# Kernel tuning notes

Measured on AMD Instinct MI355X. Metric: run time of the kernel, lower is better.

Reference implementation:

```python
import jax, jax.numpy as jnp
import numpy as np
import math

D = 512
BT = 4096
N = 16
EPS = 1e-5

def layer_norm(x, g, b):
    mu = jnp.mean(x, axis=-1, keepdims=True)
    var = jnp.mean(jnp.square(x - mu), axis=-1, keepdims=True)
    return (x - mu) * jax.lax.rsqrt(var + EPS) * g + b

def setup_inputs() -> dict:
    key = jax.random.key(0)
    ks = jax.random.split(key, 8)
    x = jax.random.normal(ks[0], (BT, N, D), dtype=jnp.float32)
    # random bool mask (True = masked), but keep the diagonal unmasked so no
    # row is fully -inf (avoids NaN softmax, matching sane usage of the module)
    attn_mask = jax.random.randint(ks[1], (BT, N, N), 0, 2).astype(bool)
    eye = jnp.eye(N, dtype=bool)[None, :, :]
    attn_mask = jnp.where(eye, False, attn_mask)
    # LayerNorm params (torch init: weight=1, bias=0)
    g1 = jnp.ones((D,), jnp.float32); b1 = jnp.zeros((D,), jnp.float32)
    g2 = jnp.ones((D,), jnp.float32); b2 = jnp.zeros((D,), jnp.float32)
    # FFN params: Linear(D, 4D) then Linear(4D, D)
    s1 = 1.0 / math.sqrt(D)
    s2 = 1.0 / math.sqrt(4 * D)
    W1 = jax.random.uniform(ks[2], (D, 4 * D), jnp.float32, -s1, s1)
    bW1 = jax.random.uniform(ks[3], (4 * D,), jnp.float32, -s1, s1)
    W2 = jax.random.uniform(ks[4], (4 * D, D), jnp.float32, -s2, s2)
    bW2 = jax.random.uniform(ks[5], (D,), jnp.float32, -s2, s2)
    return {"x": x, "attn_mask": attn_mask, "g1": g1, "b1": b1,
            "g2": g2, "b2": b2, "W1": W1, "bW1": bW1, "W2": W2, "bW2": bW2}

def reference(x, attn_mask, g1, b1, g2, b2, W1, bW1, W2, bW2):
    d = x.shape[-1]
    # scores: [BT, N, N] = x x^T / sqrt(d)
    scores = jnp.einsum('bnd,bmd->bnm', x, x) / jnp.sqrt(jnp.asarray(d, x.dtype))
    scores = jnp.where(attn_mask, -jnp.inf, scores)
    attn = jax.nn.softmax(scores, axis=-1)
    out = jnp.einsum('bnm,bmd->bnd', attn, x)
    h = layer_norm(x + out, g1, b1)
    ff = jnp.maximum(h @ W1 + bW1, 0.0) @ W2 + bW2
    y = layer_norm(h + ff, g2, b2)
    return y, attn
```

## Files before the change

kernel.cpp:

```cpp
#include <hip/hip_runtime.h>

typedef float  f32x4 __attribute__((ext_vector_type(4)));
typedef short  short8 __attribute__((ext_vector_type(8)));

__device__ __forceinline__ unsigned short f2bf(float f) {
    unsigned u = __builtin_bit_cast(unsigned, f);
    unsigned r = u + 0x7FFFu + ((u >> 16) & 1u);
    return (unsigned short)(r >> 16);
}
__device__ __forceinline__ float bf2f(unsigned short b) {
    return __builtin_bit_cast(float, (unsigned)b << 16);
}

__device__ __forceinline__ f32x4 mfma16(short8 a, short8 b, f32x4 c) {
    return __builtin_amdgcn_mfma_f32_16x16x32_bf16(a, b, c, 0, 0, 0);
}

#define GLOAD16(gp, lp) \
    __builtin_amdgcn_global_load_lds((const __attribute__((address_space(1))) unsigned int*)(gp), \
                                     (__attribute__((address_space(3))) unsigned int*)(lp), 16, 0, 0)

#define BT   4096
#define NTOK 16
#define DDIM 512
#define Y_ELEMS 33554432ULL
#define XS_STRIDE 516

__global__ __launch_bounds__(256) void transpose_kernel(const float* __restrict__ in,
                                                        unsigned short* __restrict__ out,
                                                        int R, int C) {
    __shared__ float tile[32][33];
    const int tx = threadIdx.x & 31, ty = threadIdx.x >> 5;
    const int c0 = blockIdx.x * 32, r0 = blockIdx.y * 32;
#pragma unroll
    for (int i = 0; i < 4; ++i)
        tile[ty + 8 * i][tx] = in[(size_t)(r0 + ty + 8 * i) * C + c0 + tx];
    __syncthreads();
#pragma unroll
    for (int i = 0; i < 4; ++i)
        out[(size_t)(c0 + ty + 8 * i) * R + r0 + tx] = f2bf(tile[tx][ty + 8 * i]);
}

__global__ void detect_kernel(const unsigned char* __restrict__ m, int* __restrict__ flag) {
    __shared__ int any;
    if (threadIdx.x == 0) any = 0;
    __syncthreads();
    int loc = 0;
    for (int i = threadIdx.x; i < 4096; i += 256)
        if (i & 3) loc |= m[i];
    if (loc) atomicOr(&any, 1);
    __syncthreads();
    if (threadIdx.x == 0) *flag = any ? 1 : 0;
}

__global__ __launch_bounds__(256) void stage1_kernel(
    const float* __restrict__ x,
    const unsigned char* __restrict__ mask_u8, const int* __restrict__ mask_i32,
    const int* __restrict__ flagp,
    const float* __restrict__ g1, const float* __restrict__ b1,
    float* __restrict__ attn_out, unsigned short* __restrict__ hbf,
    float* __restrict__ hf32) {
    __shared__ float xs[NTOK * XS_STRIDE];
    __shared__ float p_lds[256];

    const int b = blockIdx.x, t = threadIdx.x;
    const float* xb = x + (size_t)b * (NTOK * DDIM);

#pragma unroll
    for (int i = 0; i < 8; ++i) {
        int s = t + 256 * i;
        int r = s >> 7, c4 = s & 127;
        f32x4 v = ((const f32x4*)xb)[s];
        *(f32x4*)(&xs[r * XS_STRIDE + c4 * 4]) = v;
    }
    __syncthreads();

    const int r = t >> 4, c = t & 15;
    {
        const f32x4* xr = (const f32x4*)(&xs[r * XS_STRIDE]);
        const f32x4* xc = (const f32x4*)(&xs[c * XS_STRIDE]);
        f32x4 d4 = {0.f, 0.f, 0.f, 0.f};
#pragma unroll 8
        for (int u = 0; u < 128; ++u) d4 += xr[u] * xc[u];
        float s_rc = (d4.x + d4.y + d4.z + d4.w) * 0.04419417382415922f;

        const int flag = *flagp;
        size_t midx = (size_t)b * 256 + t;
        bool msk = flag ? (mask_u8[midx] != 0) : (mask_i32[midx] != 0);
        float sv = msk ? -1e30f : s_rc;
        float mx = sv;
        mx = fmaxf(mx, __shfl_xor(mx, 1, 16));
        mx = fmaxf(mx, __shfl_xor(mx, 2, 16));
        mx = fmaxf(mx, __shfl_xor(mx, 4, 16));
        mx = fmaxf(mx, __shfl_xor(mx, 8, 16));
        float e = msk ? 0.f : expf(sv - mx);
        float sum = e;
        sum += __shfl_xor(sum, 1, 16);
        sum += __shfl_xor(sum, 2, 16);
        sum += __shfl_xor(sum, 4, 16);
        sum += __shfl_xor(sum, 8, 16);
        float p = e / sum;
        p_lds[t] = p;
        attn_out[midx] = p;
    }
    __syncthreads();

    const int r2 = t >> 4, tc = t & 15;
    f32x4 acc[8];
#pragma unroll
    for (int j = 0; j < 8; ++j) acc[j] = (f32x4){0.f, 0.f, 0.f, 0.f};
    for (int c2 = 0; c2 < 16; ++c2) {
        float pw = p_lds[r2 * 16 + c2];
        const f32x4* xrow = (const f32x4*)(&xs[c2 * XS_STRIDE]);
#pragma unroll
        for (int j = 0; j < 8; ++j) acc[j] += pw * xrow[tc + 16 * j];
    }

    const f32x4* xme = (const f32x4*)(&xs[r2 * XS_STRIDE]);
    f32x4 vv[8];
    float s1 = 0.f, s2 = 0.f;
#pragma unroll
    for (int j = 0; j < 8; ++j) {
        f32x4 v = xme[tc + 16 * j] + acc[j];
        vv[j] = v;
        s1 += v.x + v.y + v.z + v.w;
        s2 += v.x * v.x + v.y * v.y + v.z * v.z + v.w * v.w;
    }
    s1 += __shfl_xor(s1, 1, 16); s2 += __shfl_xor(s2, 1, 16);
    s1 += __shfl_xor(s1, 2, 16); s2 += __shfl_xor(s2, 2, 16);
    s1 += __shfl_xor(s1, 4, 16); s2 += __shfl_xor(s2, 4, 16);
    s1 += __shfl_xor(s1, 8, 16); s2 += __shfl_xor(s2, 8, 16);
    float mu = s1 * (1.f / 512.f);
    float var = s2 * (1.f / 512.f) - mu * mu;
    float inv = rsqrtf(var + 1e-5f);

    const size_t rowbase = (size_t)(b * NTOK + r2) * DDIM;
    unsigned short* hrow = hbf + rowbase;
    float* frow = hf32 + rowbase;
#pragma unroll
    for (int j = 0; j < 8; ++j) {
        int u = tc + 16 * j;
        f32x4 gv = ((const f32x4*)g1)[u];
        f32x4 bv = ((const f32x4*)b1)[u];
        f32x4 o = (vv[j] - mu) * inv * gv + bv;
        *(f32x4*)(frow + u * 4) = o;
        uint2 pk;
        pk.x = (unsigned)f2bf(o.x) | ((unsigned)f2bf(o.y) << 16);
        pk.y = (unsigned)f2bf(o.z) | ((unsigned)f2bf(o.w) << 16);
        *(uint2*)(hrow + u * 4) = pk;
    }
}


#define PH_READA(Al, Q) { short8 a00, a01, a10, a11; \
    a00 = *(const short8*)((Al) + aoffs[2*(Q)]   + kk2[0]); \
    a01 = *(const short8*)((Al) + aoffs[2*(Q)]   + kk2[1]); \
    a10 = *(const short8*)((Al) + aoffs[2*(Q)+1] + kk2[0]); \
    a11 = *(const short8*)((Al) + aoffs[2*(Q)+1] + kk2[1]);

#define PH_READB(Bl) \
    bb00 = *(const short8*)((Bl) + boffs[0] + kk2[0]); \
    bb01 = *(const short8*)((Bl) + boffs[0] + kk2[1]); \
    bb10 = *(const short8*)((Bl) + boffs[1] + kk2[0]); \
    bb11 = *(const short8*)((Bl) + boffs[1] + kk2[1]); \
    bb20 = *(const short8*)((Bl) + boffs[2] + kk2[0]); \
    bb21 = *(const short8*)((Bl) + boffs[2] + kk2[1]); \
    bb30 = *(const short8*)((Bl) + boffs[3] + kk2[0]); \
    bb31 = *(const short8*)((Bl) + boffs[3] + kk2[1]);

#define PH_MFMA(Q) \
    __builtin_amdgcn_s_barrier(); \
    asm volatile("s_waitcnt lgkmcnt(0)" ::: "memory"); \
    __builtin_amdgcn_sched_barrier(0); \
    __builtin_amdgcn_s_setprio(1); \
    acc[2*(Q)][0]   = mfma16(a00, bb00, acc[2*(Q)][0]); \
    acc[2*(Q)][0]   = mfma16(a01, bb01, acc[2*(Q)][0]); \
    acc[2*(Q)][1]   = mfma16(a00, bb10, acc[2*(Q)][1]); \
    acc[2*(Q)][1]   = mfma16(a01, bb11, acc[2*(Q)][1]); \
    acc[2*(Q)][2]   = mfma16(a00, bb20, acc[2*(Q)][2]); \
    acc[2*(Q)][2]   = mfma16(a01, bb21, acc[2*(Q)][2]); \
    acc[2*(Q)][3]   = mfma16(a00, bb30, acc[2*(Q)][3]); \
    acc[2*(Q)][3]   = mfma16(a01, bb31, acc[2*(Q)][3]); \
    acc[2*(Q)+1][0] = mfma16(a10, bb00, acc[2*(Q)+1][0]); \
    acc[2*(Q)+1][0] = mfma16(a11, bb01, acc[2*(Q)+1][0]); \
    acc[2*(Q)+1][1] = mfma16(a10, bb10, acc[2*(Q)+1][1]); \
    acc[2*(Q)+1][1] = mfma16(a11, bb11, acc[2*(Q)+1][1]); \
    acc[2*(Q)+1][2] = mfma16(a10, bb20, acc[2*(Q)+1][2]); \
    acc[2*(Q)+1][2] = mfma16(a11, bb21, acc[2*(Q)+1][2]); \
    acc[2*(Q)+1][3] = mfma16(a10, bb30, acc[2*(Q)+1][3]); \
    acc[2*(Q)+1][3] = mfma16(a11, bb31, acc[2*(Q)+1][3]); \
    __builtin_amdgcn_s_setprio(0);

#define PH_END  __builtin_amdgcn_s_barrier(); }

#define GEMM_BODY(MORE) \
        PH_READA(A0lds, 0) PH_READB(B0lds) \
        stage(A, arow0, v, A1lds, 0); \
        stage(A, arow0, v, A1lds, 1); \
        PH_MFMA(0) PH_END \
        PH_READA(A0lds, 1) \
        if (MORE) stage(Bw, (size_t)n0, u2, B0lds, 0); \
        PH_MFMA(1) PH_END \
        PH_READA(A0lds, 2) \
        if (MORE) stage(Bw, (size_t)n0, u2, B0lds, 1); \
        PH_MFMA(2) PH_END \
        PH_READA(A0lds, 3) \
        PH_MFMA(3) \
        if (MORE) { asm volatile("s_waitcnt vmcnt(4)" ::: "memory"); } \
        else      { asm volatile("s_waitcnt vmcnt(0)" ::: "memory"); } \
        PH_END \
        PH_READA(A1lds, 0) PH_READB(B1lds) \
        if (MORE) stage(A, arow0, u2, A0lds, 0); \
        PH_MFMA(0) PH_END \
        PH_READA(A1lds, 1) \
        if (MORE) stage(A, arow0, u2, A0lds, 1); \
        PH_MFMA(1) PH_END \
        PH_READA(A1lds, 2) \
        if (MORE) stage(Bw, (size_t)n0, v2, B1lds, 0); \
        PH_MFMA(2) PH_END \
        PH_READA(A1lds, 3) \
        if (MORE) stage(Bw, (size_t)n0, v2, B1lds, 1); \
        PH_MFMA(3) \
        if (MORE) { asm volatile("s_waitcnt vmcnt(4)" ::: "memory"); } \
        PH_END

template <bool FFN1>
__global__ __launch_bounds__(512, 2) void gemm8_kernel(
    const unsigned short* __restrict__ A, const unsigned short* __restrict__ Bw,
    const float* __restrict__ bias, unsigned short* __restrict__ Cbf,
    float* Cf, long out_row0) {
    constexpr int K   = FFN1 ? 512 : 2048;
    constexpr int NT  = K / 64;
    constexpr int NXT = FFN1 ? 8 : 2;
    constexpr int NC  = FFN1 ? 2048 : 512;

    extern __shared__ unsigned short lds[];
    unsigned short* A0lds = lds;
    unsigned short* B0lds = lds + 16384;
    unsigned short* A1lds = lds + 32768;
    unsigned short* B1lds = lds + 49152;

    const int nwg = (int)gridDim.x;
    const int orig = (int)blockIdx.x;
    const int q8 = nwg >> 3, r8 = nwg & 7;
    const int xcd = orig & 7, idx = orig >> 3;
    const int w = (xcd < r8 ? xcd * (q8 + 1) : r8 * (q8 + 1) + (xcd - r8) * q8) + idx;
    const int mt_i = w / NXT, nt_i = w % NXT;
    const size_t arow0 = (size_t)mt_i * 256;
    const int n0 = nt_i * 256;

    const int tid = threadIdx.x;
    const int l = tid & 63, wv = tid >> 6;
    const int wm = wv >> 2, wn = wv & 3;
    const int lr = l & 15, lq = l >> 4;

    const int srow = tid >> 3;
    const int skb  = ((((tid & 7) << 4) ^ ((srow & 7) << 4)) >> 1);

    const int sw = (lr & 7) << 4;
    int kk2[2];
    kk2[0] = ((lq * 16) ^ sw) >> 1;
    kk2[1] = ((64 + lq * 16) ^ sw) >> 1;
    int aoffs[8], boffs[4];
#pragma unroll
    for (int mf = 0; mf < 8; ++mf) aoffs[mf] = (wm * 128 + mf * 16 + lr) * 64;
#pragma unroll
    for (int nf = 0; nf < 4; ++nf) boffs[nf] = (wn * 64 + nf * 16 + lr) * 64;

    f32x4 acc[8][4];
#pragma unroll
    for (int i = 0; i < 8; ++i)
#pragma unroll
        for (int j = 0; j < 4; ++j) acc[i][j] = (f32x4){0.f, 0.f, 0.f, 0.f};

    short8 bb00, bb01, bb10, bb11, bb20, bb21, bb30, bb31;

    auto stage = [&](const unsigned short* gb, size_t rbase, int tile, unsigned short* dst, int half) {
        const unsigned short* g = gb + (rbase + (size_t)(half * 128 + srow)) * K + tile * 64 + skb;
        unsigned short* d = dst + half * 8192 + tid * 8;
        GLOAD16(g, d);
        GLOAD16(g + (size_t)64 * K, d + 4096);
    };

    stage(Bw, (size_t)n0, 0, B0lds, 0);
    stage(Bw, (size_t)n0, 0, B0lds, 1);
    stage(A,  arow0,      0, A0lds, 0);
    stage(A,  arow0,      0, A0lds, 1);
    stage(Bw, (size_t)n0, 1, B1lds, 0);
    stage(Bw, (size_t)n0, 1, B1lds, 1);
    asm volatile("s_waitcnt vmcnt(4)" ::: "memory");
    __builtin_amdgcn_s_barrier();

#pragma unroll 1
    for (int t = 0; t < NT / 2 - 1; ++t) {
        const int v = 2 * t + 1, u2 = 2 * t + 2, v2 = 2 * t + 3;
        GEMM_BODY(1)
    }
    {
        const int t = NT / 2 - 1;
        const int v = 2 * t + 1, u2 = 2 * t + 2, v2 = 2 * t + 3;
        (void)u2; (void)v2;
        GEMM_BODY(0)
    }

    float bv[4];
#pragma unroll
    for (int nf = 0; nf < 4; ++nf) bv[nf] = bias[n0 + wn * 64 + nf * 16 + lr];

#pragma unroll
    for (int mf = 0; mf < 8; ++mf) {
#pragma unroll
        for (int qq = 0; qq < 4; ++qq) {
            long row = (long)arow0 + wm * 128 + mf * 16 + lq * 4 + qq;
            if (FFN1) {
#pragma unroll
                for (int nf = 0; nf < 4; ++nf) {
                    int col = n0 + wn * 64 + nf * 16 + lr;
                    float vvv = acc[mf][nf][qq] + bv[nf];
                    Cbf[(size_t)row * NC + col] = f2bf(fmaxf(vvv, 0.f));
                }
            } else {
                long grow = out_row0 + row;
#pragma unroll
                for (int nf = 0; nf < 4; ++nf) {
                    int col = n0 + wn * 64 + nf * 16 + lr;
                    size_t gidx = (size_t)grow * 512 + col;
                    Cf[gidx] = acc[mf][nf][qq] + bv[nf] + Cf[gidx];
                }
            }
        }
    }
}

__global__ __launch_bounds__(256) void ln2_kernel(float* __restrict__ zy,
                                                  const float* __restrict__ g2,
                                                  const float* __restrict__ b2) {
    const int row = blockIdx.x * 4 + (threadIdx.x >> 6);
    const int l = threadIdx.x & 63;
    f32x4* rp = (f32x4*)(zy + (size_t)row * 512);
    f32x4 v0 = rp[l], v1 = rp[l + 64];
    float s = v0.x + v0.y + v0.z + v0.w + v1.x + v1.y + v1.z + v1.w;
    float s2 = v0.x * v0.x + v0.y * v0.y + v0.z * v0.z + v0.w * v0.w +
               v1.x * v1.x + v1.y * v1.y + v1.z * v1.z + v1.w * v1.w;
#pragma unroll
    for (int d = 1; d < 64; d <<= 1) {
        s += __shfl_xor(s, d, 64);
        s2 += __shfl_xor(s2, d, 64);
    }
    float mu = s * (1.f / 512.f);
    float var = s2 * (1.f / 512.f) - mu * mu;
    float inv = rsqrtf(var + 1e-5f);
    f32x4 ga = ((const f32x4*)g2)[l], gb = ((const f32x4*)g2)[l + 64];
    f32x4 ba = ((const f32x4*)b2)[l], bb = ((const f32x4*)b2)[l + 64];
    rp[l] = (v0 - mu) * inv * ga + ba;
    rp[l + 64] = (v1 - mu) * inv * gb + bb;
}

extern "C" void kernel_launch(void* const* d_in, const int* in_sizes, int n_in,
                              void* d_out, int out_size, void* d_ws, size_t ws_size,
                              hipStream_t stream) {
    const float* x = (const float*)d_in[0];
    const void* mask = d_in[1];
    const float* g1 = (const float*)d_in[2];
    const float* b1 = (const float*)d_in[3];
    const float* g2 = (const float*)d_in[4];
    const float* b2 = (const float*)d_in[5];
    const float* W1 = (const float*)d_in[6];
    const float* bW1 = (const float*)d_in[7];
    const float* W2 = (const float*)d_in[8];
    const float* bW2 = (const float*)d_in[9];

    float* y = (float*)d_out;
    float* attn = y + Y_ELEMS;
    char* ws = (char*)d_ws;
    unsigned short* W1T = (unsigned short*)(ws);
    unsigned short* W2T = (unsigned short*)(ws + 2097152);
    int* flag = (int*)(ws + 4194304);
    unsigned short* h = (unsigned short*)(ws + 4194560);
    unsigned short* t1 = (unsigned short*)(ws + 71303424ULL);

    hipFuncSetAttribute((const void*)gemm8_kernel<true>,
                        hipFuncAttributeMaxDynamicSharedMemorySize, 131072);
    hipFuncSetAttribute((const void*)gemm8_kernel<false>,
                        hipFuncAttributeMaxDynamicSharedMemorySize, 131072);

    long cap256 = ((long)ws_size - 71303424L) / (256L * 2048L * 2L);
    if (cap256 < 1) cap256 = 1;
    if (cap256 > 256) cap256 = 256;

    transpose_kernel<<<dim3(64, 16), dim3(256), 0, stream>>>(W1, W1T, 512, 2048);
    transpose_kernel<<<dim3(16, 64), dim3(256), 0, stream>>>(W2, W2T, 2048, 512);
    detect_kernel<<<1, 256, 0, stream>>>((const unsigned char*)mask, flag);
    stage1_kernel<<<4096, 256, 0, stream>>>(x, (const unsigned char*)mask, (const int*)mask,
                                            flag, g1, b1, attn, h, y);
    for (long t0 = 0; t0 < 256; t0 += cap256) {
        long mt = (256 - t0 < cap256) ? (256 - t0) : cap256;
        long row0 = t0 * 256;
        gemm8_kernel<true><<<dim3((unsigned)(8 * mt)), 512, 131072, stream>>>(
            h + (size_t)row0 * 512, W1T, bW1, t1, nullptr, 0);
        gemm8_kernel<false><<<dim3((unsigned)(2 * mt)), 512, 131072, stream>>>(
            t1, W2T, bW2, nullptr, y, row0);
    }
    ln2_kernel<<<16384, 256, 0, stream>>>(y, g2, b2);
}
```

Baseline: 445.7 us.

## Fuse second LayerNorm into FFN2 GEMM epilogue with full-row tiles

FFN2 GEMM now uses 128x512 tiles so each block owns whole rows. The epilogue adds bias and a bf16 residual from h, then applies LayerNorm2 via a cross-wave LDS reduction. This removes the fp32 h write in stage1, the read-modify-write of y and the separate ln2 kernel. The cost is a larger LDS footprint (160KB), likely lower occupancy, and a residual taken at bf16 precision.

```diff
diff --git a/kernel.cpp b/kernel.cpp
--- a/kernel.cpp
+++ b/kernel.cpp
@@ -58,8 +58,7 @@
     const unsigned char* __restrict__ mask_u8, const int* __restrict__ mask_i32,
     const int* __restrict__ flagp,
     const float* __restrict__ g1, const float* __restrict__ b1,
-    float* __restrict__ attn_out, unsigned short* __restrict__ hbf,
-    float* __restrict__ hf32) {
+    float* __restrict__ attn_out, unsigned short* __restrict__ hbf) {
     __shared__ float xs[NTOK * XS_STRIDE];
     __shared__ float p_lds[256];
 
@@ -134,23 +133,19 @@
     float var = s2 * (1.f / 512.f) - mu * mu;
     float inv = rsqrtf(var + 1e-5f);
 
-    const size_t rowbase = (size_t)(b * NTOK + r2) * DDIM;
-    unsigned short* hrow = hbf + rowbase;
-    float* frow = hf32 + rowbase;
+    unsigned short* hrow = hbf + (size_t)(b * NTOK + r2) * DDIM;
 #pragma unroll
     for (int j = 0; j < 8; ++j) {
         int u = tc + 16 * j;
         f32x4 gv = ((const f32x4*)g1)[u];
         f32x4 bv = ((const f32x4*)b1)[u];
         f32x4 o = (vv[j] - mu) * inv * gv + bv;
-        *(f32x4*)(frow + u * 4) = o;
         uint2 pk;
         pk.x = (unsigned)f2bf(o.x) | ((unsigned)f2bf(o.y) << 16);
         pk.y = (unsigned)f2bf(o.z) | ((unsigned)f2bf(o.w) << 16);
         *(uint2*)(hrow + u * 4) = pk;
     }
 }
-
 
 #define PH_READA(Al, Q) { short8 a00, a01, a10, a11; \
     a00 = *(const short8*)((Al) + aoffs[2*(Q)]   + kk2[0]); \
@@ -224,15 +219,13 @@
         if (MORE) { asm volatile("s_waitcnt vmcnt(4)" ::: "memory"); } \
         PH_END
 
-template <bool FFN1>
-__global__ __launch_bounds__(512, 2) void gemm8_kernel(
+__global__ __launch_bounds__(512, 2) void gemm1_kernel(
     const unsigned short* __restrict__ A, const unsigned short* __restrict__ Bw,
-    const float* __restrict__ bias, unsigned short* __restrict__ Cbf,
-    float* Cf, long out_row0) {
-    constexpr int K   = FFN1 ? 512 : 2048;
-    constexpr int NT  = K / 64;
-    constexpr int NXT = FFN1 ? 8 : 2;
-    constexpr int NC  = FFN1 ? 2048 : 512;
+    const float* __restrict__ bias, unsigned short* __restrict__ Cbf) {
+    constexpr int K = 512;
+    constexpr int NT = K / 64;
+    constexpr int NXT = 8;
+    constexpr int NC = 2048;
 
     extern __shared__ unsigned short lds[];
     unsigned short* A0lds = lds;
@@ -255,7 +248,7 @@
     const int lr = l & 15, lq = l >> 4;
 
     const int srow = tid >> 3;
-    const int skb  = ((((tid & 7) << 4) ^ ((srow & 7) << 4)) >> 1);
+    const int skb = ((((tid & 7) << 4) ^ ((srow & 7) << 4)) >> 1);
 
     const int sw = (lr & 7) << 4;
     int kk2[2];
@@ -312,48 +305,196 @@
 #pragma unroll
         for (int qq = 0; qq < 4; ++qq) {
             long row = (long)arow0 + wm * 128 + mf * 16 + lq * 4 + qq;
-            if (FFN1) {
-#pragma unroll
-                for (int nf = 0; nf < 4; ++nf) {
-                    int col = n0 + wn * 64 + nf * 16 + lr;
-                    float vvv = acc[mf][nf][qq] + bv[nf];
-                    Cbf[(size_t)row * NC + col] = f2bf(fmaxf(vvv, 0.f));
-                }
-            } else {
-                long grow = out_row0 + row;
-#pragma unroll
-                for (int nf = 0; nf < 4; ++nf) {
-                    int col = n0 + wn * 64 + nf * 16 + lr;
-                    size_t gidx = (size_t)grow * 512 + col;
-                    Cf[gidx] = acc[mf][nf][qq] + bv[nf] + Cf[gidx];
-                }
+#pragma unroll
+            for (int nf = 0; nf < 4; ++nf) {
+                int col = n0 + wn * 64 + nf * 16 + lr;
+                float vvv = acc[mf][nf][qq] + bv[nf];
+                Cbf[(size_t)row * NC + col] = f2bf(fmaxf(vvv, 0.f));
             }
         }
     }
 }
 
-__global__ __launch_bounds__(256) void ln2_kernel(float* __restrict__ zy,
-                                                  const float* __restrict__ g2,
-                                                  const float* __restrict__ b2) {
-    const int row = blockIdx.x * 4 + (threadIdx.x >> 6);
-    const int l = threadIdx.x & 63;
-    f32x4* rp = (f32x4*)(zy + (size_t)row * 512);
-    f32x4 v0 = rp[l], v1 = rp[l + 64];
-    float s = v0.x + v0.y + v0.z + v0.w + v1.x + v1.y + v1.z + v1.w;
-    float s2 = v0.x * v0.x + v0.y * v0.y + v0.z * v0.z + v0.w * v0.w +
-               v1.x * v1.x + v1.y * v1.y + v1.z * v1.z + v1.w * v1.w;
-#pragma unroll
-    for (int d = 1; d < 64; d <<= 1) {
-        s += __shfl_xor(s, d, 64);
-        s2 += __shfl_xor(s2, d, 64);
-    }
-    float mu = s * (1.f / 512.f);
-    float var = s2 * (1.f / 512.f) - mu * mu;
-    float inv = rsqrtf(var + 1e-5f);
-    f32x4 ga = ((const f32x4*)g2)[l], gb = ((const f32x4*)g2)[l + 64];
-    f32x4 ba = ((const f32x4*)b2)[l], bb = ((const f32x4*)b2)[l + 64];
-    rp[l] = (v0 - mu) * inv * ga + ba;
-    rp[l + 64] = (v1 - mu) * inv * gb + bb;
+
+#define Q2_READB(Bl) \
+    _Pragma("unroll") \
+    for (int nf = 0; nf < 8; ++nf) { \
+        bb[2 * nf]     = *(const short8*)((Bl) + boffs2[nf] + kk2[0]); \
+        bb[2 * nf + 1] = *(const short8*)((Bl) + boffs2[nf] + kk2[1]); \
+    }
+
+#define Q2_PH(Al, Q) { short8 a0_, a1_; \
+    a0_ = *(const short8*)((Al) + aoffs2[Q] + kk2[0]); \
+    a1_ = *(const short8*)((Al) + aoffs2[Q] + kk2[1]);
+
+#define Q2_MFMA(Q) \
+    __builtin_amdgcn_s_barrier(); \
+    asm volatile("s_waitcnt lgkmcnt(0)" ::: "memory"); \
+    __builtin_amdgcn_sched_barrier(0); \
+    __builtin_amdgcn_s_setprio(1); \
+    _Pragma("unroll") \
+    for (int nf = 0; nf < 8; ++nf) { \
+        acc[Q][nf] = mfma16(a0_, bb[2 * nf],     acc[Q][nf]); \
+        acc[Q][nf] = mfma16(a1_, bb[2 * nf + 1], acc[Q][nf]); \
+    } \
+    __builtin_amdgcn_s_setprio(0);
+
+#define Q2_END  __builtin_amdgcn_s_barrier(); }
+
+#define BODY2(MORE) \
+        Q2_READB(B0l) \
+        Q2_PH(A0l, 0) stageA(v, A1l); Q2_MFMA(0) Q2_END \
+        Q2_PH(A0l, 1) if (MORE) stageB(u2, B0l, 0); Q2_MFMA(1) Q2_END \
+        Q2_PH(A0l, 2) if (MORE) stageB(u2, B0l, 1); Q2_MFMA(2) Q2_END \
+        Q2_PH(A0l, 3) Q2_MFMA(3) \
+        if (MORE) { asm volatile("s_waitcnt vmcnt(8)" ::: "memory"); } \
+        else      { asm volatile("s_waitcnt vmcnt(0)" ::: "memory"); } \
+        Q2_END \
+        Q2_READB(B1l) \
+        Q2_PH(A1l, 0) if (MORE) stageA(u2, A0l); Q2_MFMA(0) Q2_END \
+        Q2_PH(A1l, 1) if (MORE) stageB(v2, B1l, 0); Q2_MFMA(1) Q2_END \
+        Q2_PH(A1l, 2) if (MORE) stageB(v2, B1l, 1); Q2_MFMA(2) Q2_END \
+        Q2_PH(A1l, 3) Q2_MFMA(3) \
+        if (MORE) { asm volatile("s_waitcnt vmcnt(8)" ::: "memory"); } \
+        Q2_END
+
+__global__ __launch_bounds__(512, 2) void gemm2ln_kernel(
+    const unsigned short* __restrict__ A,
+    const unsigned short* __restrict__ Bw,
+    const float* __restrict__ bias,
+    const unsigned short* __restrict__ hres,
+    const float* __restrict__ g2, const float* __restrict__ b2,
+    float* __restrict__ y, long out_row0) {
+    constexpr int K = 2048;
+    constexpr int NT = K / 64;
+
+    extern __shared__ unsigned short lds[];
+    unsigned short* A0l = lds;
+    unsigned short* A1l = lds + 8192;
+    unsigned short* B0l = lds + 16384;
+    unsigned short* B1l = lds + 49152;
+
+    const int nwg = (int)gridDim.x;
+    const int orig = (int)blockIdx.x;
+    const int q8 = nwg >> 3, r8 = nwg & 7;
+    const int xcd = orig & 7, idx = orig >> 3;
+    const int w = (xcd < r8 ? xcd * (q8 + 1) : r8 * (q8 + 1) + (xcd - r8) * q8) + idx;
+    const size_t arow0 = (size_t)w * 128;
+
+    const int tid = threadIdx.x;
+    const int l = tid & 63, wv = tid >> 6;
+    const int wm = wv & 1, wn = wv >> 1;
+    const int lr = l & 15, lq = l >> 4;
+
+    const int srow = tid >> 3;
+    const int skb = ((((tid & 7) << 4) ^ ((srow & 7) << 4)) >> 1);
+
+    const int sw = (lr & 7) << 4;
+    int kk2[2];
+    kk2[0] = ((lq * 16) ^ sw) >> 1;
+    kk2[1] = ((64 + lq * 16) ^ sw) >> 1;
+    int aoffs2[4], boffs2[8];
+#pragma unroll
+    for (int mf = 0; mf < 4; ++mf) aoffs2[mf] = (wm * 64 + mf * 16 + lr) * 64;
+#pragma unroll
+    for (int nf = 0; nf < 8; ++nf) boffs2[nf] = (wn * 128 + nf * 16 + lr) * 64;
+
+    f32x4 acc[4][8];
+#pragma unroll
+    for (int i = 0; i < 4; ++i)
+#pragma unroll
+        for (int j = 0; j < 8; ++j) acc[i][j] = (f32x4){0.f, 0.f, 0.f, 0.f};
+
+    short8 bb[16];
+
+    auto stageA = [&](int tile, unsigned short* dst) {
+        const unsigned short* g = A + (arow0 + srow) * K + tile * 64 + skb;
+        unsigned short* d = dst + tid * 8;
+        GLOAD16(g, d);
+        GLOAD16(g + (size_t)64 * K, d + 4096);
+    };
+    auto stageB = [&](int tile, unsigned short* dst, int half) {
+        const unsigned short* g = Bw + (size_t)(half * 256 + srow) * K + tile * 64 + skb;
+        unsigned short* d = dst + half * 16384 + tid * 8;
+#pragma unroll
+        for (int i = 0; i < 4; ++i)
+            GLOAD16(g + (size_t)(64 * i) * K, d + 4096 * i);
+    };
+
+    stageB(0, B0l, 0);
+    stageB(0, B0l, 1);
+    stageA(0, A0l);
+    stageB(1, B1l, 0);
+    stageB(1, B1l, 1);
+    asm volatile("s_waitcnt vmcnt(8)" ::: "memory");
+    __builtin_amdgcn_s_barrier();
+
+#pragma unroll 1
+    for (int t = 0; t < NT / 2 - 1; ++t) {
+        const int v = 2 * t + 1, u2 = 2 * t + 2, v2 = 2 * t + 3;
+        BODY2(1)
+    }
+    {
+        const int t = NT / 2 - 1;
+        const int v = 2 * t + 1, u2 = 2 * t + 2, v2 = 2 * t + 3;
+        (void)u2; (void)v2;
+        BODY2(0)
+    }
+
+    float* red = (float*)lds;
+    float bv2[8], gv2[8], bb2[8];
+#pragma unroll
+    for (int nf = 0; nf < 8; ++nf) {
+        int col = wn * 128 + nf * 16 + lr;
+        bv2[nf] = bias[col];
+        gv2[nf] = g2[col];
+        bb2[nf] = b2[col];
+    }
+
+#pragma unroll
+    for (int mf = 0; mf < 4; ++mf) {
+#pragma unroll
+        for (int qq = 0; qq < 4; ++qq) {
+            int lrow = wm * 64 + mf * 16 + lq * 4 + qq;
+            long grow = out_row0 + (long)arow0 + lrow;
+            const unsigned short* hr = hres + (size_t)grow * 512 + wn * 128 + lr;
+            float s = 0.f, s2 = 0.f;
+#pragma unroll
+            for (int nf = 0; nf < 8; ++nf) {
+                float z = acc[mf][nf][qq] + bv2[nf] + bf2f(hr[nf * 16]);
+                acc[mf][nf][qq] = z;
+                s += z;
+                s2 += z * z;
+            }
+            s += __shfl_xor(s, 1, 16); s2 += __shfl_xor(s2, 1, 16);
+            s += __shfl_xor(s, 2, 16); s2 += __shfl_xor(s2, 2, 16);
+            s += __shfl_xor(s, 4, 16); s2 += __shfl_xor(s2, 4, 16);
+            s += __shfl_xor(s, 8, 16); s2 += __shfl_xor(s2, 8, 16);
+            if (lr == 0) {
+                red[wn * 128 + lrow] = s;
+                red[512 + wn * 128 + lrow] = s2;
+            }
+        }
+    }
+    __syncthreads();
+
+#pragma unroll
+    for (int mf = 0; mf < 4; ++mf) {
+#pragma unroll
+        for (int qq = 0; qq < 4; ++qq) {
+            int lrow = wm * 64 + mf * 16 + lq * 4 + qq;
+            long grow = out_row0 + (long)arow0 + lrow;
+            float s = red[lrow] + red[128 + lrow] + red[256 + lrow] + red[384 + lrow];
+            float s2 = red[512 + lrow] + red[640 + lrow] + red[768 + lrow] + red[896 + lrow];
+            float mu = s * (1.f / 512.f);
+            float var = s2 * (1.f / 512.f) - mu * mu;
+            float inv = rsqrtf(var + 1e-5f);
+            float* yr = y + (size_t)grow * 512 + wn * 128 + lr;
+#pragma unroll
+            for (int nf = 0; nf < 8; ++nf)
+                yr[nf * 16] = (acc[mf][nf][qq] - mu) * inv * gv2[nf] + bb2[nf];
+        }
+    }
 }
 
 extern "C" void kernel_launch(void* const* d_in, const int* in_sizes, int n_in,
@@ -379,10 +520,10 @@
     unsigned short* h = (unsigned short*)(ws + 4194560);
     unsigned short* t1 = (unsigned short*)(ws + 71303424ULL);
 
-    hipFuncSetAttribute((const void*)gemm8_kernel<true>,
+    hipFuncSetAttribute((const void*)gemm1_kernel,
                         hipFuncAttributeMaxDynamicSharedMemorySize, 131072);
-    hipFuncSetAttribute((const void*)gemm8_kernel<false>,
-                        hipFuncAttributeMaxDynamicSharedMemorySize, 131072);
+    hipFuncSetAttribute((const void*)gemm2ln_kernel,
+                        hipFuncAttributeMaxDynamicSharedMemorySize, 163840);
 
     long cap256 = ((long)ws_size - 71303424L) / (256L * 2048L * 2L);
     if (cap256 < 1) cap256 = 1;
@@ -392,14 +533,13 @@
     transpose_kernel<<<dim3(16, 64), dim3(256), 0, stream>>>(W2, W2T, 2048, 512);
     detect_kernel<<<1, 256, 0, stream>>>((const unsigned char*)mask, flag);
     stage1_kernel<<<4096, 256, 0, stream>>>(x, (const unsigned char*)mask, (const int*)mask,
-                                            flag, g1, b1, attn, h, y);
+                                            flag, g1, b1, attn, h);
     for (long t0 = 0; t0 < 256; t0 += cap256) {
         long mt = (256 - t0 < cap256) ? (256 - t0) : cap256;
         long row0 = t0 * 256;
-        gemm8_kernel<true><<<dim3((unsigned)(8 * mt)), 512, 131072, stream>>>(
-            h + (size_t)row0 * 512, W1T, bW1, t1, nullptr, 0);
-        gemm8_kernel<false><<<dim3((unsigned)(2 * mt)), 512, 131072, stream>>>(
-            t1, W2T, bW2, nullptr, y, row0);
-    }
-    ln2_kernel<<<16384, 256, 0, stream>>>(y, g2, b2);
-}
+        gemm1_kernel<<<dim3((unsigned)(8 * mt)), 512, 131072, stream>>>(
+            h + (size_t)row0 * 512, W1T, bW1, t1);
+        gemm2ln_kernel<<<dim3((unsigned)(2 * mt)), 512, 163840, stream>>>(
+            t1, W2T, bW2, h, g2, b2, y, row0);
+    }
+}
```

After: 411.3 us. 7.7% less time.
